# Optimization experiments

Hardware: AMD Instinct MI355X
Metric: run time of the kernel (lower is better)

Reference implementation:

```python
import jax, jax.numpy as jnp
import numpy as np

IN_FEATURES = 8192
OUT_FEATURES = 14336
M_TOKENS = 64


def _dequant_rowwise_int4(w_packed, w_scales):
    # w_packed: [out, in//2], each byte holds two signed int4 values
    # (low nibble = even k index, high nibble = odd k index, two's complement)
    low = w_packed & 0xF
    high = (w_packed >> 4) & 0xF
    q = jnp.stack([low, high], axis=-1).reshape(w_packed.shape[0], -1)  # [out, in]
    q = jnp.where(q >= 8, q - 16, q).astype(jnp.float32)
    return q * w_scales[:, None]  # [out, in]


def setup_inputs() -> dict:
    key = jax.random.key(0)
    k1, k2, k3, k4 = jax.random.split(key, 4)
    x = jax.random.normal(k1, (M_TOKENS, IN_FEATURES), dtype=jnp.float32)
    w_packed = jax.random.randint(k2, (OUT_FEATURES, IN_FEATURES // 2), 0, 256, dtype=jnp.int32)
    # per-row scales, small positive values as produced by max-abs/7 quantization
    w_scales = jax.random.uniform(k3, (OUT_FEATURES,), dtype=jnp.float32) * 0.02 + 1e-4
    bias = jax.random.normal(k4, (OUT_FEATURES,), dtype=jnp.float32)
    return {"x": x, "w_packed": w_packed, "w_scales": w_scales, "bias": bias}


def reference(x, w_packed, w_scales, bias):
    original_shape = x.shape[:-1]
    x_2d = x.reshape(-1, IN_FEATURES)
    w = _dequant_rowwise_int4(w_packed, w_scales)  # [out, in]
    y = x_2d @ w.T + bias[None, :]  # [M, out]
    return y.reshape(*original_shape, OUT_FEATURES)
```

## Files before the change

### kernel.cpp

```cpp
#include <hip/hip_runtime.h>

#define IN_F   8192
#define OUT_F  14336
#define M_TOK  64
#define KPI    4096
#define BN     128
#define NBLK   (OUT_F / BN)
#define KSPLIT 16
#define KCHUNK (IN_F / KSPLIT)
#define PSTRIDE (M_TOK * OUT_F)

typedef __attribute__((ext_vector_type(8)))  short bf16x8;
typedef __attribute__((ext_vector_type(16))) float f32x16;

__device__ __forceinline__ unsigned short f2bf_rne(float f) {
    unsigned u = __builtin_bit_cast(unsigned, f);
    u += 0x7FFFu + ((u >> 16) & 1u);
    return (unsigned short)(u >> 16);
}

__global__ __launch_bounds__(256) void qlin_prep(const float* __restrict__ x,
                                                 unsigned short* __restrict__ xb) {
    int gid = blockIdx.x * 256 + threadIdx.x;
    float4 v = reinterpret_cast<const float4*>(x)[gid];
    ushort4 o;
    o.x = f2bf_rne(v.x);
    o.y = f2bf_rne(v.y);
    o.z = f2bf_rne(v.z);
    o.w = f2bf_rne(v.w);
    reinterpret_cast<ushort4*>(xb)[gid] = o;
}

__device__ __forceinline__ int unpack2_bf16(int v) {
    int q0 = ((int)((unsigned)v << 28)) >> 28;
    int q1 = ((int)((unsigned)v << 24)) >> 28;
    unsigned u0 = __builtin_bit_cast(unsigned, (float)q0);
    unsigned u1 = __builtin_bit_cast(unsigned, (float)q1);
    return (int)((u0 >> 16) | (u1 & 0xFFFF0000u));
}

__device__ __forceinline__ bf16x8 unpack_b(int4 wv) {
    int4 pk;
    pk.x = unpack2_bf16(wv.x);
    pk.y = unpack2_bf16(wv.y);
    pk.z = unpack2_bf16(wv.z);
    pk.w = unpack2_bf16(wv.w);
    return __builtin_bit_cast(bf16x8, pk);
}

__global__ __launch_bounds__(256) void qlin_gemm(const unsigned short* __restrict__ xb,
                                                 const int* __restrict__ wp,
                                                 const float* __restrict__ scales,
                                                 float* __restrict__ part) {
    const int tid  = threadIdx.x;
    const int wave = tid >> 6;
    const int lane = tid & 63;
    const int tp   = lane & 31;
    const int qp   = lane >> 5;

    const int nblk = blockIdx.x % NBLK;
    const int kblk = blockIdx.x / NBLK;
    const int n0   = nblk * BN;
    const int n    = n0 + wave * 32 + tp;
    const int kb   = kblk * KCHUNK;

    const int4*   wrow = reinterpret_cast<const int4*>(wp + (size_t)n * KPI + (kb >> 1));
    const bf16x8* x0   = reinterpret_cast<const bf16x8*>(xb + (size_t)tp * IN_F + kb);
    const bf16x8* x1   = reinterpret_cast<const bf16x8*>(xb + (size_t)(32 + tp) * IN_F + kb);

    f32x16 acc0 = {0.f,0.f,0.f,0.f,0.f,0.f,0.f,0.f,0.f,0.f,0.f,0.f,0.f,0.f,0.f,0.f};
    f32x16 acc1 = acc0;

#pragma unroll 4
    for (int s = 0; s < KCHUNK / 16; ++s) {
        const int idx = s * 2 + qp;
        int4   wv = wrow[idx];
        bf16x8 a0 = x0[idx];
        bf16x8 a1 = x1[idx];
        bf16x8 b  = unpack_b(wv);
        acc0 = __builtin_amdgcn_mfma_f32_32x32x16_bf16(a0, b, acc0, 0, 0, 0);
        acc1 = __builtin_amdgcn_mfma_f32_32x32x16_bf16(a1, b, acc1, 0, 0, 0);
    }

    const float sc = scales[n];
    float* p = part + (size_t)kblk * PSTRIDE;
#pragma unroll
    for (int reg = 0; reg < 16; ++reg) {
        int m = (reg & 3) + 8 * (reg >> 2) + 4 * qp;
        p[(size_t)m        * OUT_F + n] = acc0[reg] * sc;
        p[(size_t)(32 + m) * OUT_F + n] = acc1[reg] * sc;
    }
}

__global__ __launch_bounds__(256) void qlin_reduce(const float* __restrict__ part,
                                                   const float* __restrict__ bias,
                                                   float* __restrict__ out) {
    int g = blockIdx.x * 256 + threadIdx.x;
    float4 acc = reinterpret_cast<const float4*>(bias)[g % (OUT_F / 4)];
#pragma unroll
    for (int s = 0; s < KSPLIT; ++s) {
        float4 v = reinterpret_cast<const float4*>(part + (size_t)s * PSTRIDE)[g];
        acc.x += v.x; acc.y += v.y; acc.z += v.z; acc.w += v.w;
    }
    reinterpret_cast<float4*>(out)[g] = acc;
}

extern "C" void kernel_launch(void* const* d_in, const int* in_sizes, int n_in,
                              void* d_out, int out_size, void* d_ws, size_t ws_size,
                              hipStream_t stream) {
    const float* x    = (const float*)d_in[0];
    const int*   wp   = (const int*)d_in[1];
    const float* sc   = (const float*)d_in[2];
    const float* bias = (const float*)d_in[3];
    float* out = (float*)d_out;

    unsigned short* xb   = (unsigned short*)d_ws;
    float*          part = (float*)((char*)d_ws + (1 << 20));

    qlin_prep<<<(M_TOK * IN_F) / 4 / 256, 256, 0, stream>>>(x, xb);
    qlin_gemm<<<NBLK * KSPLIT, 256, 0, stream>>>(xb, wp, sc, part);
    qlin_reduce<<<(M_TOK * OUT_F) / 4 / 256, 256, 0, stream>>>(part, bias, out);
}
```

Before: 400.0 us.

## Stage weights and activations through double-buffered LDS with async global loads

The GEMM kernel now copies weight and activation tiles into XOR-swizzled shared-memory double buffers using global_load_lds, and overlaps the copy of the next tile with the MFMA compute on the current one. Before, each lane read its operands straight from global memory. The K split is cut from 16 to 8, which halves the partial-sum traffic the reduce kernel has to read, at the cost of fewer blocks for parallelism. The reduce kernel is relaunched on a 2D grid, and the hand-written waitcnt counts and barriers have to match the number of outstanding loads exactly.

New measurement: 354.1 us. 11.5% less time.

```diff
diff --git a/kernel.cpp b/kernel.cpp
--- a/kernel.cpp
+++ b/kernel.cpp
@@ -6,8 +6,10 @@
 #define KPI    4096
 #define BN     128
 #define NBLK   (OUT_F / BN)
-#define KSPLIT 16
+#define KSPLIT 8
 #define KCHUNK (IN_F / KSPLIT)
+#define BK     64
+#define NSTEP  (KCHUNK / BK)
 #define PSTRIDE (M_TOK * OUT_F)
 
 typedef __attribute__((ext_vector_type(8)))  short bf16x8;
@@ -48,10 +50,20 @@
     return __builtin_bit_cast(bf16x8, pk);
 }
 
+__device__ __forceinline__ void gload_lds16(const void* g, void* l) {
+    __builtin_amdgcn_global_load_lds(
+        (const __attribute__((address_space(1))) unsigned int*)g,
+        (__attribute__((address_space(3))) unsigned int*)l,
+        16, 0, 0);
+}
+
 __global__ __launch_bounds__(256) void qlin_gemm(const unsigned short* __restrict__ xb,
                                                  const int* __restrict__ wp,
                                                  const float* __restrict__ scales,
                                                  float* __restrict__ part) {
+    __shared__ int            wlds[2][BN * (BK / 2)];
+    __shared__ unsigned short xlds[2][M_TOK * BK];
+
     const int tid  = threadIdx.x;
     const int wave = tid >> 6;
     const int lane = tid & 63;
@@ -61,27 +73,69 @@
     const int nblk = blockIdx.x % NBLK;
     const int kblk = blockIdx.x / NBLK;
     const int n0   = nblk * BN;
-    const int n    = n0 + wave * 32 + tp;
     const int kb   = kblk * KCHUNK;
-
-    const int4*   wrow = reinterpret_cast<const int4*>(wp + (size_t)n * KPI + (kb >> 1));
-    const bf16x8* x0   = reinterpret_cast<const bf16x8*>(xb + (size_t)tp * IN_F + kb);
-    const bf16x8* x1   = reinterpret_cast<const bf16x8*>(xb + (size_t)(32 + tp) * IN_F + kb);
 
     f32x16 acc0 = {0.f,0.f,0.f,0.f,0.f,0.f,0.f,0.f,0.f,0.f,0.f,0.f,0.f,0.f,0.f,0.f};
     f32x16 acc1 = acc0;
 
-#pragma unroll 4
-    for (int s = 0; s < KCHUNK / 16; ++s) {
-        const int idx = s * 2 + qp;
-        int4   wv = wrow[idx];
-        bf16x8 a0 = x0[idx];
-        bf16x8 a1 = x1[idx];
-        bf16x8 b  = unpack_b(wv);
-        acc0 = __builtin_amdgcn_mfma_f32_32x32x16_bf16(a0, b, acc0, 0, 0, 0);
-        acc1 = __builtin_amdgcn_mfma_f32_32x32x16_bf16(a1, b, acc1, 0, 0, 0);
+#define STAGE(b, t) do {                                                           \
+    _Pragma("unroll")                                                              \
+    for (int j = 0; j < 4; ++j) {                                                  \
+        int li = (wave * 4 + j) * 64 + lane;                     \
+        int r  = li >> 3;                                   \
+        int cg = (li & 7) ^ (r & 7);                  \
+        const int* gp = wp + (size_t)(n0 + r) * KPI + (kb >> 1) + (t) * (BK / 2) + cg * 4; \
+        gload_lds16(gp, (char*)&wlds[b][0] + (size_t)li * 16);                     \
+    }                                                                              \
+    _Pragma("unroll")                                                              \
+    for (int j = 0; j < 2; ++j) {                                                  \
+        int li = (wave * 2 + j) * 64 + lane;                      \
+        int r  = li >> 3;                                         \
+        int cg = (li & 7) ^ (r & 7);                                               \
+        const unsigned short* gp = xb + (size_t)r * IN_F + kb + (t) * BK + cg * 8; \
+        gload_lds16(gp, (char*)&xlds[b][0] + (size_t)li * 16);                     \
+    }                                                                              \
+} while (0)
+
+#define COMPUTE(b) do {                                                            \
+    _Pragma("unroll")                                                              \
+    for (int kf = 0; kf < 4; ++kf) {                                               \
+        const int c = kf * 2 + qp;                      \
+        const int R = wave * 32 + tp;                                              \
+        int4 wv = *reinterpret_cast<const int4*>(                                  \
+            (const char*)&wlds[b][0] + (size_t)(R * 8 + (c ^ (R & 7))) * 16);      \
+        bf16x8 bb = unpack_b(wv);                                                  \
+        bf16x8 a0 = *reinterpret_cast<const bf16x8*>(                              \
+            (const char*)&xlds[b][0] + (size_t)(tp * 8 + (c ^ (tp & 7))) * 16);    \
+        bf16x8 a1 = *reinterpret_cast<const bf16x8*>(                              \
+            (const char*)&xlds[b][0] + (size_t)((32 + tp) * 8 + (c ^ (tp & 7))) * 16); \
+        acc0 = __builtin_amdgcn_mfma_f32_32x32x16_bf16(a0, bb, acc0, 0, 0, 0);     \
+        acc1 = __builtin_amdgcn_mfma_f32_32x32x16_bf16(a1, bb, acc1, 0, 0, 0);     \
+    }                                                                              \
+} while (0)
+
+    STAGE(0, 0);
+    STAGE(1, 1);
+
+    for (int t = 0; t < NSTEP - 1; ++t) {
+        const int cur = t & 1;
+        asm volatile("s_waitcnt vmcnt(6)" ::: "memory");
+        __builtin_amdgcn_sched_barrier(0);
+        __builtin_amdgcn_s_barrier();
+        __builtin_amdgcn_sched_barrier(0);
+        COMPUTE(cur);
+        __builtin_amdgcn_sched_barrier(0);
+        __builtin_amdgcn_s_barrier();
+        __builtin_amdgcn_sched_barrier(0);
+        if (t + 2 < NSTEP) STAGE(cur, t + 2);
     }
+    asm volatile("s_waitcnt vmcnt(0)" ::: "memory");
+    __builtin_amdgcn_sched_barrier(0);
+    __builtin_amdgcn_s_barrier();
+    __builtin_amdgcn_sched_barrier(0);
+    COMPUTE((NSTEP - 1) & 1);
 
+    const int   n  = n0 + wave * 32 + tp;
     const float sc = scales[n];
     float* p = part + (size_t)kblk * PSTRIDE;
 #pragma unroll
@@ -90,19 +144,23 @@
         p[(size_t)m        * OUT_F + n] = acc0[reg] * sc;
         p[(size_t)(32 + m) * OUT_F + n] = acc1[reg] * sc;
     }
+#undef STAGE
+#undef COMPUTE
 }
 
 __global__ __launch_bounds__(256) void qlin_reduce(const float* __restrict__ part,
                                                    const float* __restrict__ bias,
                                                    float* __restrict__ out) {
-    int g = blockIdx.x * 256 + threadIdx.x;
-    float4 acc = reinterpret_cast<const float4*>(bias)[g % (OUT_F / 4)];
+    const int    nq   = blockIdx.x * 256 + threadIdx.x;
+    const int    m    = blockIdx.y;
+    const size_t base = (size_t)m * (OUT_F / 4) + nq;
+    float4 acc = reinterpret_cast<const float4*>(bias)[nq];
 #pragma unroll
     for (int s = 0; s < KSPLIT; ++s) {
-        float4 v = reinterpret_cast<const float4*>(part + (size_t)s * PSTRIDE)[g];
+        float4 v = reinterpret_cast<const float4*>(part)[(size_t)s * (PSTRIDE / 4) + base];
         acc.x += v.x; acc.y += v.y; acc.z += v.z; acc.w += v.w;
     }
-    reinterpret_cast<float4*>(out)[g] = acc;
+    reinterpret_cast<float4*>(out)[base] = acc;
 }
 
 extern "C" void kernel_launch(void* const* d_in, const int* in_sizes, int n_in,
@@ -119,5 +177,5 @@
 
     qlin_prep<<<(M_TOK * IN_F) / 4 / 256, 256, 0, stream>>>(x, xb);
     qlin_gemm<<<NBLK * KSPLIT, 256, 0, stream>>>(xb, wp, sc, part);
-    qlin_reduce<<<(M_TOK * OUT_F) / 4 / 256, 256, 0, stream>>>(part, bias, out);
+    qlin_reduce<<<dim3(OUT_F / 4 / 256, M_TOK), 256, 0, stream>>>(part, bias, out);
 }
```
